# Kernel tuning notes

Hardware: AMD Instinct MI355X
Metric: run time of the kernel (lower is better)

Reference implementation:

```python
import jax, jax.numpy as jnp
import numpy as np

B, S, D = 2, 2048, 4096
H, HD = 32, 128  # heads, head_dim
ROPE_BASE = 10000.0


def setup_inputs() -> dict:
    key = jax.random.key(0)
    k1, k2, k3 = jax.random.split(key, 3)
    positions = jnp.broadcast_to(jnp.arange(S, dtype=jnp.int64), (B, S))
    hidden_states = jax.random.normal(k1, (B, S, D), dtype=jnp.float32)
    W_qkv = jax.random.normal(k2, (D, 3 * D), dtype=jnp.float32) * (D ** -0.5)
    W_o = jax.random.normal(k3, (D, D), dtype=jnp.float32) * (D ** -0.5)
    return {"positions": positions, "hidden_states": hidden_states, "W_qkv": W_qkv, "W_o": W_o}


def _apply_rope(x, positions):
    # x: [B,S,H,HD]; neox-style rotate-half RoPE
    half = HD // 2
    inv_freq = 1.0 / (ROPE_BASE ** (jnp.arange(0, half, dtype=jnp.float32) / half))
    ang = positions.astype(jnp.float32)[..., None] * inv_freq  # [B,S,half]
    cos = jnp.cos(ang)[:, :, None, :]  # [B,S,1,half]
    sin = jnp.sin(ang)[:, :, None, :]
    x1, x2 = x[..., :half], x[..., half:]
    return jnp.concatenate([x1 * cos - x2 * sin, x2 * cos + x1 * sin], axis=-1)


def reference(positions, hidden_states, W_qkv, W_o):
    qkv = jnp.einsum('bsd,de->bse', hidden_states, W_qkv)
    q, k, v = jnp.split(qkv, 3, axis=-1)
    q = q.reshape(B, S, H, HD)
    k = k.reshape(B, S, H, HD)
    v = v.reshape(B, S, H, HD)
    q = _apply_rope(q, positions)
    k = _apply_rope(k, positions)
    scale = HD ** -0.5
    scores = jnp.einsum('bqhd,bkhd->bhqk', q, k) * scale
    causal = jnp.tril(jnp.ones((S, S), dtype=bool))
    scores = jnp.where(causal[None, None], scores, jnp.finfo(scores.dtype).min)
    probs = jax.nn.softmax(scores, axis=-1)
    attn = jnp.einsum('bhqk,bkhd->bqhd', probs, v).reshape(B, S, D)
    return jnp.einsum('bsd,de->bse', attn, W_o)
```

## Files before the change

kernel.cpp:

```cpp
#include <hip/hip_runtime.h>
#include <hip/hip_bf16.h>
#include <stdint.h>

typedef unsigned short u16;
typedef __attribute__((ext_vector_type(8))) short short8;
typedef __attribute__((ext_vector_type(4))) float f32x4;

__device__ __forceinline__ float bf2f(u16 u) {
  union { uint32_t i; float f; } v; v.i = ((uint32_t)u) << 16; return v.f;
}
__device__ __forceinline__ u16 f2bf(float x) {
  union { float f; uint32_t i; } v; v.f = x;
  uint32_t r = v.i + 0x7FFFu + ((v.i >> 16) & 1u);
  return (u16)(r >> 16);
}
__device__ __forceinline__ void gld16(const void* g, void* l) {
  __builtin_amdgcn_global_load_lds((const __attribute__((address_space(1))) void*)g,
                                   (__attribute__((address_space(3))) void*)l, 16, 0, 0);
}


__global__ __launch_bounds__(256) void cvt_bf16_k(const float* __restrict__ in, u16* __restrict__ out, int n) {
  int i = (blockIdx.x * 256 + threadIdx.x) * 4;
  int stride = gridDim.x * 256 * 4;
  for (; i < n; i += stride) {
    float4 v = *(const float4*)(in + i);
    ushort4 o;
    o.x = f2bf(v.x); o.y = f2bf(v.y); o.z = f2bf(v.z); o.w = f2bf(v.w);
    *(ushort4*)(out + i) = o;
  }
}

__global__ __launch_bounds__(256) void transpose_cvt_k(const float* __restrict__ W, u16* __restrict__ Wt,
                                                        int Kd, int Nd) {
  __shared__ float lds[64][68];
  int t = threadIdx.x;
  int n0 = blockIdx.x * 64, k0 = blockIdx.y * 64;
  int kr = t >> 2, cq = (t & 3) * 16;
  const float* src = W + (size_t)(k0 + kr) * Nd + n0 + cq;
  float4 a = *(const float4*)(src);
  float4 b = *(const float4*)(src + 4);
  float4 c = *(const float4*)(src + 8);
  float4 d = *(const float4*)(src + 12);
  *(float4*)&lds[kr][cq]      = a;
  *(float4*)&lds[kr][cq + 4]  = b;
  *(float4*)&lds[kr][cq + 8]  = c;
  *(float4*)&lds[kr][cq + 12] = d;
  __syncthreads();
  int rn = t >> 2, ks = (t & 3) * 16;
  u16 tmp[16];
  #pragma unroll
  for (int j = 0; j < 16; ++j) tmp[j] = f2bf(lds[ks + j][rn]);
  u16* dst = Wt + (size_t)(n0 + rn) * Kd + k0 + ks;
  *(short8*)dst       = *(short8*)tmp;
  *(short8*)(dst + 8) = *(short8*)(tmp + 8);
}

__global__ __launch_bounds__(64) void rope_table_k(const int* __restrict__ pos, float* __restrict__ tab) {
  int m = blockIdx.x * 64 + threadIdx.x;
  float p = (float)pos[m];
  for (int i = 0; i < 64; ++i) {
    float inv = expf(-(float)i * (9.210340371976184f / 64.0f));
    float sn, cs;
    sincosf(p * inv, &sn, &cs);
    tab[i * 4096 + m] = cs;
    tab[(64 + i) * 4096 + m] = sn;
  }
}


__device__ __forceinline__ void stage_half(const u16* __restrict__ G, u16* S, int K,
                                           int tile, int half, int w, int sr, int scsw) {
  int d = tile & 1;
  int sm = half * 8 + w;
  const u16* g = G + (size_t)(sm * 16 + sr) * K + (tile << 6) + scsw;
  u16* s = S + (size_t)(d * 32 + sm * 2) * 512;
  gld16(g, s);
  gld16(g + 32, s + 512);
}

__device__ __forceinline__ short8 frag(const u16* S, int d, int sidx, int kk, int fo) {
  return *(const short8*)&S[(size_t)((d * 32 + sidx * 2 + kk) * 512) + fo];
}

template <int MODE>
__global__ __launch_bounds__(512) void gemm256_k(const u16* __restrict__ A, const u16* __restrict__ Bt,
                                                 void* __restrict__ Cp, int N, int K, int GX,
                                                 const float* __restrict__ tab,
                                                 u16* __restrict__ Qb, u16* __restrict__ Kb,
                                                 u16* __restrict__ Vt) {
  __shared__ u16 As[2 * 32 * 512];
  __shared__ u16 Bs[2 * 32 * 512];
  int lid = blockIdx.x;
  int GY = gridDim.x / GX;
  int SY = GY >> 1, SX = GX >> 2;
  int xcd = lid & 7, idx = lid >> 3;
  int ry = xcd >> 2, rx = xcd & 3;
  int bxl = idx / SY, byl = idx - bxl * SY;
  int by = ry * SY + byl, bx = rx * SX + bxl;
  int bm0 = by << 8, bn0 = bx << 8;
  int tid = threadIdx.x, w = tid >> 6, l = tid & 63;
  int wr = w >> 2, wc = w & 3;
  const u16* Ag = A + (size_t)bm0 * K;
  const u16* Bg = Bt + (size_t)bn0 * K;
  int NT = K >> 6;
  int sr = l >> 2;
  int scsw = ((l & 3) * 8) ^ ((sr & 8) ? 16 : 0);
  int fr = l & 15;
  int g = l >> 4;
  int fo = fr * 32 + ((g * 8) ^ ((fr & 8) ? 16 : 0));

  f32x4 acc[8][4];
  #pragma unroll
  for (int i = 0; i < 8; ++i)
    #pragma unroll
    for (int j = 0; j < 4; ++j) acc[i][j] = (f32x4){0.f, 0.f, 0.f, 0.f};

  stage_half(Ag, As, K, 0, 0, w, sr, scsw);
  stage_half(Ag, As, K, 0, 1, w, sr, scsw);
  stage_half(Bg, Bs, K, 0, 0, w, sr, scsw);
  stage_half(Bg, Bs, K, 0, 1, w, sr, scsw);
  stage_half(Ag, As, K, 1, 0, w, sr, scsw);
  asm volatile("s_waitcnt vmcnt(2)" ::: "memory");
  __builtin_amdgcn_s_barrier();
  __builtin_amdgcn_sched_barrier(0);

  for (int t = 0; t < NT; ++t) {
    int d = t & 1;
    short8 a_lo[4][2], a_hi[4][2], b_lo[2][2], b_hi[2][2];
    #pragma unroll
    for (int fm = 0; fm < 4; ++fm) {
      a_lo[fm][0] = frag(As, d, wr * 8 + fm, 0, fo);
      a_lo[fm][1] = frag(As, d, wr * 8 + fm, 1, fo);
    }
    #pragma unroll
    for (int fn = 0; fn < 2; ++fn) {
      b_lo[fn][0] = frag(Bs, d, wc * 4 + fn, 0, fo);
      b_lo[fn][1] = frag(Bs, d, wc * 4 + fn, 1, fo);
    }
    if (t + 1 < NT) stage_half(Ag, As, K, t + 1, 1, w, sr, scsw);
    __builtin_amdgcn_s_barrier();
    __builtin_amdgcn_s_setprio(1);
    #pragma unroll
    for (int fm = 0; fm < 4; ++fm)
      #pragma unroll
      for (int fn = 0; fn < 2; ++fn) {
        acc[fm][fn] = __builtin_amdgcn_mfma_f32_16x16x32_bf16(a_lo[fm][0], b_lo[fn][0], acc[fm][fn], 0, 0, 0);
        acc[fm][fn] = __builtin_amdgcn_mfma_f32_16x16x32_bf16(a_lo[fm][1], b_lo[fn][1], acc[fm][fn], 0, 0, 0);
      }
    __builtin_amdgcn_s_setprio(0);
    __builtin_amdgcn_s_barrier();
    #pragma unroll
    for (int fn = 0; fn < 2; ++fn) {
      b_hi[fn][0] = frag(Bs, d, wc * 4 + 2 + fn, 0, fo);
      b_hi[fn][1] = frag(Bs, d, wc * 4 + 2 + fn, 1, fo);
    }
    if (t + 1 < NT) stage_half(Bg, Bs, K, t + 1, 0, w, sr, scsw);
    __builtin_amdgcn_s_barrier();
    __builtin_amdgcn_s_setprio(1);
    #pragma unroll
    for (int fm = 0; fm < 4; ++fm)
      #pragma unroll
      for (int fn = 0; fn < 2; ++fn) {
        acc[fm][2 + fn] = __builtin_amdgcn_mfma_f32_16x16x32_bf16(a_lo[fm][0], b_hi[fn][0], acc[fm][2 + fn], 0, 0, 0);
        acc[fm][2 + fn] = __builtin_amdgcn_mfma_f32_16x16x32_bf16(a_lo[fm][1], b_hi[fn][1], acc[fm][2 + fn], 0, 0, 0);
      }
    __builtin_amdgcn_s_setprio(0);
    __builtin_amdgcn_s_barrier();
    #pragma unroll
    for (int fm = 0; fm < 4; ++fm) {
      a_hi[fm][0] = frag(As, d, wr * 8 + 4 + fm, 0, fo);
      a_hi[fm][1] = frag(As, d, wr * 8 + 4 + fm, 1, fo);
    }
    if (t + 1 < NT) stage_half(Bg, Bs, K, t + 1, 1, w, sr, scsw);
    __builtin_amdgcn_s_barrier();
    __builtin_amdgcn_s_setprio(1);
    #pragma unroll
    for (int fm = 0; fm < 4; ++fm)
      #pragma unroll
      for (int fn = 0; fn < 2; ++fn) {
        acc[4 + fm][2 + fn] = __builtin_amdgcn_mfma_f32_16x16x32_bf16(a_hi[fm][0], b_hi[fn][0], acc[4 + fm][2 + fn], 0, 0, 0);
        acc[4 + fm][2 + fn] = __builtin_amdgcn_mfma_f32_16x16x32_bf16(a_hi[fm][1], b_hi[fn][1], acc[4 + fm][2 + fn], 0, 0, 0);
      }
    __builtin_amdgcn_s_setprio(0);
    __builtin_amdgcn_s_barrier();
    if (t + 2 < NT) stage_half(Ag, As, K, t + 2, 0, w, sr, scsw);
    __builtin_amdgcn_s_setprio(1);
    #pragma unroll
    for (int fm = 0; fm < 4; ++fm)
      #pragma unroll
      for (int fn = 0; fn < 2; ++fn) {
        acc[4 + fm][fn] = __builtin_amdgcn_mfma_f32_16x16x32_bf16(a_hi[fm][0], b_lo[fn][0], acc[4 + fm][fn], 0, 0, 0);
        acc[4 + fm][fn] = __builtin_amdgcn_mfma_f32_16x16x32_bf16(a_hi[fm][1], b_lo[fn][1], acc[4 + fm][fn], 0, 0, 0);
      }
    __builtin_amdgcn_s_setprio(0);
    if (t + 2 < NT) asm volatile("s_waitcnt vmcnt(2)" ::: "memory");
    else            asm volatile("s_waitcnt vmcnt(0)" ::: "memory");
    __builtin_amdgcn_s_barrier();
    __builtin_amdgcn_sched_barrier(0);
  }

  if (MODE == 1) {
    int r0 = bm0 + wr * 128 + (g << 2);
    int c0 = bn0 + wc * 64 + fr;
    #pragma unroll
    for (int fm = 0; fm < 8; ++fm)
      #pragma unroll
      for (int fn = 0; fn < 4; ++fn)
        #pragma unroll
        for (int r = 0; r < 4; ++r) {
          size_t idx2 = (size_t)(r0 + fm * 16 + r) * N + (c0 + fn * 16);
          ((float*)Cp)[idx2] = acc[fm][fn][r];
        }
  } else {
    int seg = bn0 >> 12;
    int cb_base = bn0 & 4095;
    int b_ = bm0 >> 11;
    int s_base = bm0 & 2047;
    int g4 = g << 2;
    if (seg < 2) {
      float qs = (seg == 0) ? 0.08838834764831845f : 1.0f;
      u16* dstb = (seg == 0) ? Qb : Kb;
      float* xch = (float*)As;
      #pragma unroll 1
      for (int fm = 0; fm < 8; ++fm) {
        #pragma unroll
        for (int fn = 0; fn < 4; ++fn)
          #pragma unroll
          for (int r = 0; r < 4; ++r)
            xch[(w * 16 + g4 + r) * 65 + fn * 16 + fr] = acc[fm][fn][r];
        __syncthreads();
        #pragma unroll
        for (int fn = 0; fn < 4; ++fn) {
          int cb = wc * 64 + fn * 16 + fr;
          int d = cb & 127;
          int hh = (cb_base + cb) >> 7;
          int i = d & 63;
          int srow = s_base + wr * 128 + fm * 16 + g4;
          int mbase = b_ * 2048 + srow;
          float4 cs4 = *(const float4*)&tab[(size_t)i * 4096 + mbase];
          float4 sn4 = *(const float4*)&tab[(size_t)(64 + i) * 4096 + mbase];
          u16* dst = dstb + ((size_t)(b_ * 32 + hh) * 2048 + srow) * 128 + d;
          float csa[4] = {cs4.x, cs4.y, cs4.z, cs4.w};
          float sna[4] = {sn4.x, sn4.y, sn4.z, sn4.w};
          #pragma unroll
          for (int r = 0; r < 4; ++r) {
            float own = acc[fm][fn][r];
            float part = xch[((w ^ 1) * 16 + g4 + r) * 65 + fn * 16 + fr];
            float val = (d < 64) ? (own * csa[r] - part * sna[r]) : (own * csa[r] + part * sna[r]);
            dst[(size_t)r * 128] = f2bf(val * qs);
          }
        }
        __syncthreads();
      }
    } else {
      #pragma unroll
      for (int fm = 0; fm < 8; ++fm)
        #pragma unroll
        for (int fn = 0; fn < 4; ++fn) {
          int cb = wc * 64 + fn * 16 + fr;
          int d = cb & 127;
          int hh = (cb_base + cb) >> 7;
          int srow = s_base + wr * 128 + fm * 16 + g4;
          ushort4 t4;
          t4.x = f2bf(acc[fm][fn][0]); t4.y = f2bf(acc[fm][fn][1]);
          t4.z = f2bf(acc[fm][fn][2]); t4.w = f2bf(acc[fm][fn][3]);
          *(ushort4*)(Vt + (size_t)(b_ * 32 + hh) * (128 * 2048) + (size_t)d * 2048 + srow) = t4;
        }
    }
  }
}


__device__ __forceinline__ void stage_kv(const u16* __restrict__ Kg, const u16* __restrict__ Vg,
                                         u16* Ksb, u16* Vsb, int j0, int w, int l) {
  #pragma unroll
  for (int c = 0; c < 2; ++c) {
    int rk = c * 32 + w * 4 + (l >> 4);
    int kcol = ((l & 15) * 8) ^ ((rk & 7) << 3);
    gld16(Kg + (size_t)(j0 + rk) * 128 + kcol, Ksb + (c * 32 + w * 4) * 128);
    int rv = c * 64 + w * 8 + (l >> 3);
    int vcol = ((l & 7) * 8) ^ ((rv & 7) << 3);
    gld16(Vg + (size_t)rv * 2048 + j0 + vcol, Vsb + (c * 64 + w * 8) * 64);
  }
}

__global__ __launch_bounds__(512, 2) void attn_k(const u16* __restrict__ Qb, const u16* __restrict__ Kb,
                                                  const u16* __restrict__ Vt, u16* __restrict__ attnb) {
  __shared__ u16 Ks[2][64 * 128];
  __shared__ u16 Vs[2][128 * 64];
  __shared__ u16 Ps[8][32 * 64];
  int lid = blockIdx.x + gridDim.x * blockIdx.y;
  int xcd = lid & 7, idx = lid >> 3;
  int bh = xcd * 8 + (idx & 7);
  int qt = 7 - (idx >> 3);
  int b = bh >> 5, h = bh & 31;
  int q0 = qt * 256;
  int t = threadIdx.x, w = t >> 6, l = t & 63;
  int g = l >> 4, fr = l & 15;
  const u16* Qg = Qb + (size_t)bh * (2048 * 128);
  const u16* Kg = Kb + (size_t)bh * (2048 * 128);
  const u16* Vg = Vt + (size_t)bh * (128 * 2048);

  short8 aq[2][4];
  #pragma unroll
  for (int fm = 0; fm < 2; ++fm)
    #pragma unroll
    for (int kk = 0; kk < 4; ++kk)
      aq[fm][kk] = *(const short8*)&Qg[(size_t)(q0 + w * 32 + fm * 16 + fr) * 128 + kk * 32 + g * 8];

  stage_kv(Kg, Vg, Ks[0], Vs[0], 0, w, l);
  __syncthreads();

  f32x4 zero = {0.f, 0.f, 0.f, 0.f};
  f32x4 o[2][8];
  #pragma unroll
  for (int fm = 0; fm < 2; ++fm)
    #pragma unroll
    for (int fd = 0; fd < 8; ++fd) o[fm][fd] = zero;
  float m_run[2][4], l_run[2][4];
  #pragma unroll
  for (int fm = 0; fm < 2; ++fm)
    #pragma unroll
    for (int r = 0; r < 4; ++r) { m_run[fm][r] = -1e30f; l_run[fm][r] = 0.f; }

  int NJ = 4 * qt + 4;
  for (int j = 0; j < NJ; ++j) {
    int j0 = j * 64;
    int cur = j & 1;
    if (j + 1 < NJ) stage_kv(Kg, Vg, Ks[cur ^ 1], Vs[cur ^ 1], j0 + 64, w, l);
    if (j0 < q0 + w * 32 + 32) {
      f32x4 sc[2][4];
      #pragma unroll
      for (int fm = 0; fm < 2; ++fm)
        #pragma unroll
        for (int fn = 0; fn < 4; ++fn) sc[fm][fn] = zero;
      __builtin_amdgcn_s_setprio(1);
      #pragma unroll
      for (int kk = 0; kk < 4; ++kk) {
        #pragma unroll
        for (int fn = 0; fn < 4; ++fn) {
          short8 bk = *(const short8*)&Ks[cur][(fn * 16 + fr) * 128 + ((kk * 32 + g * 8) ^ ((fr & 7) << 3))];
          #pragma unroll
          for (int fm = 0; fm < 2; ++fm)
            sc[fm][fn] = __builtin_amdgcn_mfma_f32_16x16x32_bf16(aq[fm][kk], bk, sc[fm][fn], 0, 0, 0);
        }
      }
      __builtin_amdgcn_s_setprio(0);
      int qb_ = q0 + w * 32 + (g << 2);
      int kb_ = j0 + fr;
      #pragma unroll
      for (int fm = 0; fm < 2; ++fm)
        #pragma unroll
        for (int fn = 0; fn < 4; ++fn)
          #pragma unroll
          for (int r = 0; r < 4; ++r)
            if (kb_ + fn * 16 > qb_ + fm * 16 + r) sc[fm][fn][r] = -1e30f;
      float mx[2][4];
      #pragma unroll
      for (int fm = 0; fm < 2; ++fm)
        #pragma unroll
        for (int r = 0; r < 4; ++r) {
          float v = fmaxf(fmaxf(sc[fm][0][r], sc[fm][1][r]), fmaxf(sc[fm][2][r], sc[fm][3][r]));
          v = fmaxf(v, __shfl_xor(v, 1));
          v = fmaxf(v, __shfl_xor(v, 2));
          v = fmaxf(v, __shfl_xor(v, 4));
          v = fmaxf(v, __shfl_xor(v, 8));
          mx[fm][r] = v;
        }
      float scale[2][4];
      #pragma unroll
      for (int fm = 0; fm < 2; ++fm)
        #pragma unroll
        for (int r = 0; r < 4; ++r) {
          float mn = fmaxf(m_run[fm][r], mx[fm][r]);
          scale[fm][r] = __expf(m_run[fm][r] - mn);
          m_run[fm][r] = mn;
        }
      float rs[2][4];
      #pragma unroll
      for (int fm = 0; fm < 2; ++fm)
        #pragma unroll
        for (int r = 0; r < 4; ++r) {
          float acc = 0.f;
          #pragma unroll
          for (int fn = 0; fn < 4; ++fn) {
            float p = __expf(sc[fm][fn][r] - m_run[fm][r]);
            sc[fm][fn][r] = p;
            acc += p;
          }
          acc += __shfl_xor(acc, 1);
          acc += __shfl_xor(acc, 2);
          acc += __shfl_xor(acc, 4);
          acc += __shfl_xor(acc, 8);
          rs[fm][r] = acc;
        }
      #pragma unroll
      for (int fm = 0; fm < 2; ++fm)
        #pragma unroll
        for (int r = 0; r < 4; ++r) l_run[fm][r] = l_run[fm][r] * scale[fm][r] + rs[fm][r];
      #pragma unroll
      for (int fm = 0; fm < 2; ++fm)
        #pragma unroll
        for (int fd = 0; fd < 8; ++fd)
          #pragma unroll
          for (int r = 0; r < 4; ++r) o[fm][fd][r] *= scale[fm][r];
      #pragma unroll
      for (int fm = 0; fm < 2; ++fm)
        #pragma unroll
        for (int fn = 0; fn < 4; ++fn)
          #pragma unroll
          for (int r = 0; r < 4; ++r) {
            int prow = fm * 16 + (g << 2) + r;
            Ps[w][prow * 64 + ((fn * 16 + fr) ^ ((prow & 7) << 3))] = f2bf(sc[fm][fn][r]);
          }
      __builtin_amdgcn_s_setprio(1);
      #pragma unroll
      for (int kk = 0; kk < 2; ++kk) {
        short8 pa[2];
        #pragma unroll
        for (int fm = 0; fm < 2; ++fm)
          pa[fm] = *(const short8*)&Ps[w][(fm * 16 + fr) * 64 + ((kk * 32 + g * 8) ^ ((fr & 7) << 3))];
        #pragma unroll
        for (int fd = 0; fd < 8; ++fd) {
          short8 bv = *(const short8*)&Vs[cur][(fd * 16 + fr) * 64 + ((kk * 32 + g * 8) ^ ((fr & 7) << 3))];
          #pragma unroll
          for (int fm = 0; fm < 2; ++fm)
            o[fm][fd] = __builtin_amdgcn_mfma_f32_16x16x32_bf16(pa[fm], bv, o[fm][fd], 0, 0, 0);
        }
      }
      __builtin_amdgcn_s_setprio(0);
    }
    __syncthreads();
  }

  #pragma unroll
  for (int fm = 0; fm < 2; ++fm)
    #pragma unroll
    for (int r = 0; r < 4; ++r) {
      float inv = 1.0f / l_run[fm][r];
      int srow = q0 + w * 32 + fm * 16 + (g << 2) + r;
      u16* dst = attnb + (size_t)(b * 2048 + srow) * 4096 + h * 128 + fr;
      #pragma unroll
      for (int fd = 0; fd < 8; ++fd)
        dst[fd * 16] = f2bf(o[fm][fd][r] * inv);
    }
}


extern "C" void kernel_launch(void* const* d_in, const int* in_sizes, int n_in,
                              void* d_out, int out_size, void* d_ws, size_t ws_size,
                              hipStream_t stream) {
  const int*   positions = (const int*)d_in[0];
  const float* hidden    = (const float*)d_in[1];
  const float* W_qkv     = (const float*)d_in[2];
  const float* W_o       = (const float*)d_in[3];
  float* out = (float*)d_out;
  char* ws = (char*)d_ws;

  u16* Wqkv_t    = (u16*)(ws + 0);
  u16* Wo_t      = (u16*)(ws + 0);
  u16* Qb        = (u16*)(ws + 100663296);
  u16* Kb        = (u16*)(ws + 134217728);
  u16* Vt        = (u16*)(ws + 167772160);
  u16* hidden_bf = (u16*)(ws + 201326592);
  u16* attnb     = (u16*)(ws + 201326592);
  float* tab     = (float*)(ws + 234881024);

  cvt_bf16_k<<<4096, 256, 0, stream>>>(hidden, hidden_bf, 16777216);
  transpose_cvt_k<<<dim3(192, 64), 256, 0, stream>>>(W_qkv, Wqkv_t, 4096, 12288);
  rope_table_k<<<64, 64, 0, stream>>>(positions, tab);

  gemm256_k<2><<<768, 512, 0, stream>>>(hidden_bf, Wqkv_t, nullptr, 12288, 4096, 48,
                                        tab, Qb, Kb, Vt);

  transpose_cvt_k<<<dim3(64, 64), 256, 0, stream>>>(W_o, Wo_t, 4096, 4096);

  attn_k<<<dim3(8, 64), 512, 0, stream>>>(Qb, Kb, Vt, attnb);

  gemm256_k<1><<<256, 512, 0, stream>>>(attnb, Wo_t, out, 4096, 4096, 16,
                                        nullptr, nullptr, nullptr, nullptr);
}
```

Before: 927.6 us.

## Stage QKV epilogue through LDS rows for vectorized RoPE and V-transpose stores

The QKV GEMM epilogue now writes each 16-row slice of the accumulator tile as bf16 into an LDS row buffer. Threads then re-read whole rows so they can apply RoPE on contiguous 16-element chunks and issue 16-byte stores to Q/K, or gather columns to write V-transposed with 16-byte stores. The RoPE table is switched to a position-major layout so each thread's cos/sin loads are contiguous, and its kernel now uses one thread per frequency. The V path gains an LDS round-trip and extra barriers. RoPE is now applied to bf16-rounded values, which adds a little rounding error.

```diff
diff --git a/kernel.cpp b/kernel.cpp
--- a/kernel.cpp
+++ b/kernel.cpp
@@ -57,15 +57,14 @@
 }
 
 __global__ __launch_bounds__(64) void rope_table_k(const int* __restrict__ pos, float* __restrict__ tab) {
-  int m = blockIdx.x * 64 + threadIdx.x;
+  int m = blockIdx.x, i = threadIdx.x;
   float p = (float)pos[m];
-  for (int i = 0; i < 64; ++i) {
-    float inv = expf(-(float)i * (9.210340371976184f / 64.0f));
-    float sn, cs;
-    sincosf(p * inv, &sn, &cs);
-    tab[i * 4096 + m] = cs;
-    tab[(64 + i) * 4096 + m] = sn;
-  }
+  float inv = expf(-(float)i * (9.210340371976184f / 64.0f));
+  float ang = p * inv;
+  float sn, cs;
+  sincosf(ang, &sn, &cs);
+  tab[m * 128 + i] = cs;
+  tab[m * 128 + 64 + i] = sn;
 }
 
 
@@ -218,55 +217,66 @@
     int b_ = bm0 >> 11;
     int s_base = bm0 & 2047;
     int g4 = g << 2;
-    if (seg < 2) {
-      float qs = (seg == 0) ? 0.08838834764831845f : 1.0f;
-      u16* dstb = (seg == 0) ? Qb : Kb;
-      float* xch = (float*)As;
-      #pragma unroll 1
-      for (int fm = 0; fm < 8; ++fm) {
-        #pragma unroll
-        for (int fn = 0; fn < 4; ++fn)
-          #pragma unroll
-          for (int r = 0; r < 4; ++r)
-            xch[(w * 16 + g4 + r) * 65 + fn * 16 + fr] = acc[fm][fn][r];
-        __syncthreads();
-        #pragma unroll
-        for (int fn = 0; fn < 4; ++fn) {
-          int cb = wc * 64 + fn * 16 + fr;
-          int d = cb & 127;
-          int hh = (cb_base + cb) >> 7;
-          int i = d & 63;
-          int srow = s_base + wr * 128 + fm * 16 + g4;
-          int mbase = b_ * 2048 + srow;
-          float4 cs4 = *(const float4*)&tab[(size_t)i * 4096 + mbase];
-          float4 sn4 = *(const float4*)&tab[(size_t)(64 + i) * 4096 + mbase];
-          u16* dst = dstb + ((size_t)(b_ * 32 + hh) * 2048 + srow) * 128 + d;
-          float csa[4] = {cs4.x, cs4.y, cs4.z, cs4.w};
-          float sna[4] = {sn4.x, sn4.y, sn4.z, sn4.w};
-          #pragma unroll
-          for (int r = 0; r < 4; ++r) {
-            float own = acc[fm][fn][r];
-            float part = xch[((w ^ 1) * 16 + g4 + r) * 65 + fn * 16 + fr];
-            float val = (d < 64) ? (own * csa[r] - part * sna[r]) : (own * csa[r] + part * sna[r]);
-            dst[(size_t)r * 128] = f2bf(val * qs);
-          }
-        }
-        __syncthreads();
-      }
-    } else {
-      #pragma unroll
-      for (int fm = 0; fm < 8; ++fm)
-        #pragma unroll
-        for (int fn = 0; fn < 4; ++fn) {
-          int cb = wc * 64 + fn * 16 + fr;
-          int d = cb & 127;
-          int hh = (cb_base + cb) >> 7;
-          int srow = s_base + wr * 128 + fm * 16 + g4;
-          ushort4 t4;
-          t4.x = f2bf(acc[fm][fn][0]); t4.y = f2bf(acc[fm][fn][1]);
-          t4.z = f2bf(acc[fm][fn][2]); t4.w = f2bf(acc[fm][fn][3]);
-          *(ushort4*)(Vt + (size_t)(b_ * 32 + hh) * (128 * 2048) + (size_t)d * 2048 + srow) = t4;
-        }
+    float qs = (seg == 0) ? 0.08838834764831845f : 1.0f;
+    u16* dstb = (seg == 0) ? Qb : Kb;
+    u16* rowbuf = Bs;
+    int rloc = wr * 16 + g4;
+    #pragma unroll 1
+    for (int fm = 0; fm < 8; ++fm) {
+      #pragma unroll
+      for (int fn = 0; fn < 4; ++fn)
+        #pragma unroll
+        for (int r = 0; r < 4; ++r)
+          rowbuf[(rloc + r) * 264 + wc * 64 + fn * 16 + fr] = f2bf(acc[fm][fn][r]);
+      __syncthreads();
+      if (seg < 2) {
+        int rl2 = tid >> 4, c0 = (tid & 15) * 16;
+        int s = s_base + (rl2 >> 4) * 128 + fm * 16 + (rl2 & 15);
+        int d0 = c0 & 127;
+        int hh = (cb_base + c0) >> 7;
+        const u16* rb = rowbuf + rl2 * 264;
+        bool lo = d0 < 64;
+        int po = lo ? c0 + 64 : c0 - 64;
+        short8 o0 = *(const short8*)&rb[c0];
+        short8 o1 = *(const short8*)&rb[c0 + 8];
+        short8 p0 = *(const short8*)&rb[po];
+        short8 p1 = *(const short8*)&rb[po + 8];
+        const float* tm = tab + (size_t)(b_ * 2048 + s) * 128;
+        int i0 = d0 & 63;
+        float4 cs4[4], sn4[4];
+        #pragma unroll
+        for (int q = 0; q < 4; ++q) {
+          cs4[q] = *(const float4*)&tm[i0 + q * 4];
+          sn4[q] = *(const float4*)&tm[64 + i0 + q * 4];
+        }
+        short8 r0v, r1v;
+        #pragma unroll
+        for (int j = 0; j < 16; ++j) {
+          float own  = bf2f((u16)((j < 8) ? o0[j] : o1[j - 8]));
+          float part = bf2f((u16)((j < 8) ? p0[j] : p1[j - 8]));
+          float cs = ((const float*)cs4)[j];
+          float sn = ((const float*)sn4)[j];
+          float val = lo ? (own * cs - part * sn) : (own * cs + part * sn);
+          u16 bb = f2bf(val * qs);
+          if (j < 8) r0v[j] = (short)bb; else r1v[j - 8] = (short)bb;
+        }
+        u16* dst = dstb + ((size_t)(b_ * 32 + hh) * 2048 + s) * 128 + d0;
+        *(short8*)dst = r0v;
+        *(short8*)(dst + 8) = r1v;
+      } else {
+        int d2 = tid & 255, grp = tid >> 8;
+        int hh = (cb_base + d2) >> 7, dd = d2 & 127;
+        int sb2 = s_base + grp * 128 + fm * 16;
+        short8 r0v, r1v;
+        #pragma unroll
+        for (int j = 0; j < 8; ++j)  r0v[j] = (short)rowbuf[(grp * 16 + j) * 264 + d2];
+        #pragma unroll
+        for (int j = 0; j < 8; ++j)  r1v[j] = (short)rowbuf[(grp * 16 + 8 + j) * 264 + d2];
+        u16* dst = Vt + (size_t)(b_ * 32 + hh) * (128 * 2048) + (size_t)dd * 2048 + sb2;
+        *(short8*)dst = r0v;
+        *(short8*)(dst + 8) = r1v;
+      }
+      __syncthreads();
     }
   }
 }
@@ -469,7 +479,7 @@
 
   cvt_bf16_k<<<4096, 256, 0, stream>>>(hidden, hidden_bf, 16777216);
   transpose_cvt_k<<<dim3(192, 64), 256, 0, stream>>>(W_qkv, Wqkv_t, 4096, 12288);
-  rope_table_k<<<64, 64, 0, stream>>>(positions, tab);
+  rope_table_k<<<4096, 64, 0, stream>>>(positions, tab);
 
   gemm256_k<2><<<768, 512, 0, stream>>>(hidden_bf, Wqkv_t, nullptr, 12288, 4096, 48,
                                         tab, Qb, Kb, Vt);
```

Measured after the change: 886.8 us. 1.05x faster.
